# Optimization experiments

Hardware: AMD Instinct MI355X
Metric: run time of the kernel (lower is better)

The kernel has to match this reference:

```python
import jax, jax.numpy as jnp
import numpy as np

D_MODEL, D_FF = 1024, 4096
B, T = 4, 2048
K = 614  # int(d_ff * 0.15)


def setup_inputs() -> dict:
    key = jax.random.key(0)
    k1, k2, k3, k4 = jax.random.split(key, 4)
    s_in = 1.0 / np.sqrt(D_MODEL)
    s_ff = 1.0 / np.sqrt(D_FF)
    x = jax.random.normal(k1, (B, T, D_MODEL), jnp.float32)
    # torch nn.Linear default init: U(-1/sqrt(fan_in), 1/sqrt(fan_in)); weight shape [out, in]
    W1 = jax.random.uniform(k2, (D_FF, D_MODEL), jnp.float32, -s_in, s_in)
    W2 = jax.random.uniform(k3, (D_FF, D_MODEL), jnp.float32, -s_in, s_in)
    Wo = jax.random.uniform(k4, (D_MODEL, D_FF), jnp.float32, -s_ff, s_ff)
    return {"x": x, "W1": W1, "W2": W2, "Wo": Wo, "k": K}


def reference(x, W1, W2, Wo, k):
    gate = jnp.einsum('btd,fd->btf', x, W2)                 # [B,T,D_FF]
    act = jax.nn.silu(jnp.einsum('btd,fd->btf', x, W1))     # [B,T,D_FF]
    Bx, Tx, Dff = act.shape
    flat = act.reshape(Bx * Tx, Dff)
    _, topk_idx = jax.lax.top_k(flat, k)                    # [N, k]
    rows = jnp.arange(Bx * Tx)[:, None]
    mask = jnp.zeros_like(flat).at[rows, topk_idx].set(1.0).reshape(act.shape)
    sparse_act = act * mask                                  # eval-mode exact masking
    return jnp.einsum('btf,df->btd', sparse_act * gate, Wo)  # [B,T,D_MODEL]
```

## Files before the change

kernel.cpp:

```cpp
#include <hip/hip_runtime.h>
#include <stdint.h>

#define DEV __device__ __forceinline__

using f32x4  = __attribute__((ext_vector_type(4))) float;
using bf16x8 = __attribute__((ext_vector_type(8))) short;
typedef unsigned short u16;
typedef unsigned int   u32;

typedef const __attribute__((address_space(1))) void* gptr_t;
typedef __attribute__((address_space(3))) void*       lptr_t;

DEV u16 f2bf(float f) {
  union { float f; u32 u; } v; v.f = f;
  u32 lsb = (v.u >> 16) & 1u;
  v.u += 0x7fffu + lsb;
  return (u16)(v.u >> 16);
}
DEV float bf2f(u16 h) {
  union { u32 u; float f; } v; v.u = ((u32)h) << 16;
  return v.f;
}
DEV void async16(void* lds, const void* g) {
  __builtin_amdgcn_global_load_lds((gptr_t)(uintptr_t)g,
                                   (lptr_t)(u32)(uintptr_t)lds, 16, 0, 0);
}
DEV u32 fkey(float v) {
  u32 u = __float_as_uint(v);
  return u ^ ((u & 0x80000000u) ? 0xFFFFFFFFu : 0x80000000u);
}
DEV float unfkey(u32 key) {
  const u32 ub = (key & 0x80000000u) ? (key ^ 0x80000000u) : ~key;
  return __uint_as_float(ub);
}

__global__ __launch_bounds__(256) void splitall_kernel(
    const float* __restrict__ x,  const float* __restrict__ W1,
    const float* __restrict__ W2, const float* __restrict__ Wo,
    u16* __restrict__ x_hi, u16* __restrict__ x_lo,
    u16* __restrict__ W1h,  u16* __restrict__ W1l,
    u16* __restrict__ W2h,  u16* __restrict__ Woh,
    int nX, int nW, int nWo)
{
  const int i = blockIdx.x * 256 + threadIdx.x;
  const int total = nX + 2 * nW + nWo;
  if (i >= total) return;
  if (i < nX) {
    const float v = x[i];
    const u16 h = f2bf(v);
    x_hi[i] = h; x_lo[i] = f2bf(v - bf2f(h));
  } else if (i < nX + nW) {
    const int j = i - nX;
    const float v = W1[j];
    const u16 h = f2bf(v);
    W1h[j] = h; W1l[j] = f2bf(v - bf2f(h));
  } else if (i < nX + 2 * nW) {
    const int j = i - nX - nW;
    W2h[j] = f2bf(W2[j]);
  } else {
    const int j = i - nX - 2 * nW;
    Woh[j] = f2bf(Wo[j]);
  }
}

DEV void swz_block(int& bx, int& by) {
  const int gx = gridDim.x, nwg = gx * gridDim.y;
  const int lid = by * gx + bx;
  const int cpx = nwg >> 3;
  const int swz = (lid & 7) * cpx + (lid >> 3);
  bx = swz % gx; by = swz / gx;
}

template<int K, int NSEG, bool OUTBF16>
__global__ __launch_bounds__(512, 2) void gemm8p_kernel(
    const u16* __restrict__ A0, const u16* __restrict__ A1, const u16* __restrict__ A2,
    const u16* __restrict__ B0, const u16* __restrict__ B1, const u16* __restrict__ B2,
    void* __restrict__ Cout, int N)
{
  __shared__ u16 smem[65536];

  const int tid  = threadIdx.x;
  const int lane = tid & 63;
  const int wid  = tid >> 6;
  const int wm = wid >> 2, wn = wid & 3;
  int bx = blockIdx.x, by = blockIdx.y;
  swz_block(bx, by);
  const int m0 = by * 256, n0 = bx * 256;
  constexpr int TPS    = K >> 6;
  constexpr int nTiles = NSEG * TPS;
  constexpr int nIter  = nTiles / 2;

  f32x4 acc[8][4] = {};
  bf16x8 afr[4][2], bfr[2][2];

  auto stageHT = [&](int ab, int buf, int half, int ktile) {
    const int kt  = ktile < nTiles ? ktile : nTiles - 1;
    const int seg = kt / TPS;
    const int k0  = (kt - seg * TPS) << 6;
    const u16* __restrict__ src =
        ab ? (seg == 0 ? B0 : seg == 1 ? B1 : B2)
           : (seg == 0 ? A0 : seg == 1 ? A1 : A2);
    const int g0 = (ab ? n0 : m0) + half * 128;
    const int baseu = ((buf * 2 + ab) * 2 + half) * 8192;
#pragma unroll
    for (int L = 0; L < 2; ++L) {
      const int s = L * 512 + tid;
      const int r = s >> 3, cs = s & 7;
      const int csg = cs ^ (r & 7);
      async16(smem + baseu + (L * 512 + (tid & ~63)) * 8,
              src + (size_t)(g0 + r) * K + k0 + csg * 8);
    }
  };
  auto ldA = [&](int buf, int mi, int ks) -> bf16x8 {
    const int rA = wm * 128 + mi * 16 + (lane & 15);
    const int h = rA >> 7, rl = rA & 127;
    const int cs = (ks * 4 + (lane >> 4)) ^ (rl & 7);
    return *(const bf16x8*)&smem[((buf * 2 + 0) * 2 + h) * 8192 + rl * 64 + cs * 8];
  };
  auto ldB = [&](int buf, int ni, int ks) -> bf16x8 {
    const int rB = wn * 64 + ni * 16 + (lane & 15);
    const int h = rB >> 7, rl = rB & 127;
    const int cs = (ks * 4 + (lane >> 4)) ^ (rl & 7);
    return *(const bf16x8*)&smem[((buf * 2 + 1) * 2 + h) * 8192 + rl * 64 + cs * 8];
  };

  stageHT(0, 0, 0, 0); stageHT(0, 0, 1, 0);
  stageHT(1, 0, 0, 0); stageHT(1, 0, 1, 0);
  asm volatile("s_waitcnt vmcnt(0)" ::: "memory");
  __builtin_amdgcn_sched_barrier(0);
  __builtin_amdgcn_s_barrier();
  __builtin_amdgcn_sched_barrier(0);

  for (int i = 0; i < nIter; ++i) {
    const int t2 = 2 * i;
#pragma unroll
    for (int p = 0; p < 8; ++p) {
      const int pm = p & 3, bufC = p >> 2;
      const int miB = (pm >> 1) * 4, niB = (pm & 1) * 2;
      if ((pm & 1) == 0) {
#pragma unroll
        for (int m = 0; m < 4; ++m)
#pragma unroll
          for (int ks = 0; ks < 2; ++ks)
            afr[m][ks] = ldA(bufC, miB + m, ks);
      }
#pragma unroll
      for (int n = 0; n < 2; ++n)
#pragma unroll
        for (int ks = 0; ks < 2; ++ks)
          bfr[n][ks] = ldB(bufC, niB + n, ks);
      if (p == 0)      { stageHT(0, 1, 0, t2 + 1); stageHT(0, 1, 1, t2 + 1); }
      else if (p == 1) { stageHT(1, 1, 0, t2 + 1); stageHT(1, 1, 1, t2 + 1); }
      else if (p == 4) { stageHT(0, 0, 0, t2 + 2); stageHT(0, 0, 1, t2 + 2); }
      else if (p == 5) { stageHT(1, 0, 0, t2 + 2); stageHT(1, 0, 1, t2 + 2); }
      __builtin_amdgcn_sched_barrier(0);
      __builtin_amdgcn_s_barrier();
      __builtin_amdgcn_sched_barrier(0);
      __builtin_amdgcn_s_setprio(1);
#pragma unroll
      for (int m = 0; m < 4; ++m)
#pragma unroll
        for (int n = 0; n < 2; ++n)
#pragma unroll
          for (int ks = 0; ks < 2; ++ks)
            acc[miB + m][niB + n] = __builtin_amdgcn_mfma_f32_16x16x32_bf16(
                afr[m][ks], bfr[n][ks], acc[miB + m][niB + n], 0, 0, 0);
      __builtin_amdgcn_s_setprio(0);
      if (pm == 3)
        asm volatile("s_waitcnt vmcnt(0)" ::: "memory");
      __builtin_amdgcn_sched_barrier(0);
      __builtin_amdgcn_s_barrier();
      __builtin_amdgcn_sched_barrier(0);
    }
  }
  asm volatile("s_waitcnt vmcnt(0)" ::: "memory");

#pragma unroll
  for (int mi = 0; mi < 8; ++mi) {
    const int rb = m0 + wm * 128 + mi * 16 + (lane >> 4) * 4;
#pragma unroll
    for (int ni = 0; ni < 4; ++ni) {
      const int col = n0 + wn * 64 + ni * 16 + (lane & 15);
#pragma unroll
      for (int r2 = 0; r2 < 4; ++r2) {
        if constexpr (OUTBF16)
          ((u16*)Cout)[(size_t)(rb + r2) * N + col] = f2bf(acc[mi][ni][r2]);
        else
          ((float*)Cout)[(size_t)(rb + r2) * N + col] = acc[mi][ni][r2];
      }
    }
  }
}

template<int BK>
__global__ __launch_bounds__(256) void gemm_bt(
    const u16* __restrict__ A, const u16* __restrict__ B,
    float* __restrict__ C, int N, int K)
{
  constexpr int TILE = 128 * BK;
  __shared__ u16 smem[2 * TILE];
  u16* sA = smem;
  u16* sB = smem + TILE;

  const int tid  = threadIdx.x;
  const int lane = tid & 63;
  const int wave = tid >> 6;
  const int wr = wave >> 1, wc = wave & 1;
  int bx = blockIdx.x, by = blockIdx.y;
  swz_block(bx, by);
  const int m0 = by * 128, n0 = bx * 128;

  f32x4 acc[4][4] = {};
  constexpr int SPR   = BK / 8;
  constexpr int ITERS = (128 * SPR) / 256;

  for (int k0 = 0; k0 < K; k0 += BK) {
#pragma unroll
    for (int i = 0; i < ITERS; ++i) {
      const int slot = i * 256 + tid;
      const int r = slot / SPR, cc = slot % SPR;
      const int uni = (i * 256 + wave * 64) * 8;
      async16(sA + uni, A + (size_t)(m0 + r) * K + k0 + cc * 8);
      async16(sB + uni, B + (size_t)(n0 + r) * K + k0 + cc * 8);
    }
    __syncthreads();

#pragma unroll
    for (int ks = 0; ks < BK / 32; ++ks) {
      const int kb = ks * 32 + (lane >> 4) * 8;
      bf16x8 a[4], b[4];
#pragma unroll
      for (int i = 0; i < 4; ++i) {
        a[i] = *(const bf16x8*)&sA[(wr * 64 + i * 16 + (lane & 15)) * BK + kb];
        b[i] = *(const bf16x8*)&sB[(wc * 64 + i * 16 + (lane & 15)) * BK + kb];
      }
#pragma unroll
      for (int mi = 0; mi < 4; ++mi)
#pragma unroll
        for (int ni = 0; ni < 4; ++ni)
          acc[mi][ni] = __builtin_amdgcn_mfma_f32_16x16x32_bf16(a[mi], b[ni], acc[mi][ni], 0, 0, 0);
    }
    __syncthreads();
  }

#pragma unroll
  for (int mi = 0; mi < 4; ++mi) {
    const int rbase = m0 + wr * 64 + mi * 16 + (lane >> 4) * 4;
#pragma unroll
    for (int ni = 0; ni < 4; ++ni) {
      const int col = n0 + wc * 64 + ni * 16 + (lane & 15);
#pragma unroll
      for (int r2 = 0; r2 < 4; ++r2)
        C[(size_t)(rbase + r2) * N + col] = acc[mi][ni][r2];
    }
  }
}

__global__ __launch_bounds__(256) void select9_kernel(
    const float* __restrict__ z, u16* __restrict__ gs,
    const float* __restrict__ xin, const float* __restrict__ W1,
    const int* __restrict__ kptr)
{
  const int row = blockIdx.x, tid = threadIdx.x;
  const int lane = tid & 63, wave = tid >> 6;
  const int k = *kptr;

  __shared__ float xrow[1024];
  __shared__ float sact[4096];
  __shared__ unsigned char flag[4096];
  __shared__ int wsum[4];
  __shared__ int s_nb;
  __shared__ int band_idx[256];
  __shared__ u32 band_key[256];
  __shared__ float band_act[256];

  const float* zrow = z + (size_t)row * 4096;
  u16* gsrow = gs + (size_t)row * 4096;

  float zreg[16];
#pragma unroll
  for (int q = 0; q < 4; ++q) {
    const float4 v = *(const float4*)&zrow[q * 1024 + tid * 4];
    zreg[q * 4 + 0] = v.x; zreg[q * 4 + 1] = v.y;
    zreg[q * 4 + 2] = v.z; zreg[q * 4 + 3] = v.w;
  }
  *(float4*)&xrow[tid * 4] = *(const float4*)&xin[(size_t)row * 1024 + tid * 4];
  *(u32*)&flag[tid * 4] = 0u;
  *(u32*)&flag[1024 + tid * 4] = 0u;
  *(u32*)&flag[2048 + tid * 4] = 0u;
  *(u32*)&flag[3072 + tid * 4] = 0u;
  if (tid == 0) s_nb = 0;
  __syncthreads();

  u32 prefix = 0;
  for (int step = 0; step < 22; ++step) {
    const u32 c = prefix | (1u << (31 - step));
    const float zc = unfkey(c);
    int cnt = 0;
#pragma unroll
    for (int i = 0; i < 16; ++i) cnt += (zreg[i] >= zc) ? 1 : 0;
    for (int off = 32; off; off >>= 1) cnt += __shfl_xor(cnt, off);
    if (lane == 0) wsum[wave] = cnt;
    __syncthreads();
    const int tot = wsum[0] + wsum[1] + wsum[2] + wsum[3];
    if (tot >= k) prefix = c;
    __syncthreads();
  }
  const float tau = unfkey(prefix);
  const float BANDW = 8e-4f;
  const float thi = tau + BANDW, tlo = tau - BANDW;

  int cntD = 0;
#pragma unroll
  for (int q = 0; q < 4; ++q)
#pragma unroll
    for (int j = 0; j < 4; ++j) {
      const int f = q * 1024 + tid * 4 + j;
      const float zv = zreg[q * 4 + j];
      if (zv > thi) { flag[f] = 1; ++cntD; }
      else if (zv >= tlo) {
        const int p = atomicAdd(&s_nb, 1);
        if (p < 256) band_idx[p] = f;
      }
    }
  for (int off = 32; off; off >>= 1) cntD += __shfl_xor(cntD, off);
  if (lane == 0) wsum[wave] = cntD;
  __syncthreads();
  const int D = wsum[0] + wsum[1] + wsum[2] + wsum[3];
  const int nb = (s_nb < 256) ? s_nb : 256;
  const int need = k - D;

  {
    const int gi = tid >> 2, l = tid & 3;
    const int wl = lane & ~3;
    for (int i = gi; i < nb; i += 64) {
      const int f = band_idx[i];
      const float* wr = W1 + (size_t)f * 1024;
      float v = 0.f;
#pragma unroll 8
      for (int b = 0; b < 1024; b += 16) {
        float t = __fadd_rn(__fmul_rn(xrow[b + 12 + l], wr[b + 12 + l]), v);
        t = __fadd_rn(__fmul_rn(xrow[b + 8 + l],  wr[b + 8 + l]),  t);
        t = __fadd_rn(__fmul_rn(xrow[b + 4 + l],  wr[b + 4 + l]),  t);
        v = __fadd_rn(__fmul_rn(xrow[b + 0 + l],  wr[b + 0 + l]),  t);
      }
      const float c0 = __shfl(v, wl + 0);
      const float c1 = __shfl(v, wl + 1);
      const float c2 = __shfl(v, wl + 2);
      const float c3 = __shfl(v, wl + 3);
      if (l == 0) {
        const float zrep = __fadd_rn(__fadd_rn(c0, c1), __fadd_rn(c2, c3));
        const double zd = (double)zrep;
        const float a = (float)(zd / (1.0 + exp(-zd)));
        band_act[i] = a;
        band_key[i] = fkey(a);
      }
    }
  }
  __syncthreads();

  for (int i = tid; i < nb; i += 256) {
    const u32 ki = band_key[i];
    const int fi = band_idx[i];
    int rank = 0;
    for (int j = 0; j < nb; ++j) {
      const u32 kj = band_key[j];
      rank += (kj > ki || (kj == ki && band_idx[j] < fi)) ? 1 : 0;
    }
    if (rank < need) { flag[fi] = 2; sact[fi] = band_act[i]; }
  }
  __syncthreads();

#pragma unroll
  for (int q = 0; q < 4; ++q) {
    const int f0 = q * 1024 + tid * 4;
    const ushort4 gu = *(const ushort4*)&gsrow[f0];
    const float gvv[4] = { bf2f(gu.x), bf2f(gu.y), bf2f(gu.z), bf2f(gu.w) };
    const u32 fl = *(const u32*)&flag[f0];
    u16 out[4];
#pragma unroll
    for (int j = 0; j < 4; ++j) {
      const u32 fj = (fl >> (8 * j)) & 0xFF;
      float sval = 0.f;
      if (fj == 2) {
        sval = sact[f0 + j] * gvv[j];
      } else if (fj == 1) {
        const float zz = zreg[q * 4 + j];
        sval = (zz / (1.f + expf(-zz))) * gvv[j];
      }
      out[j] = f2bf(sval);
    }
    *(ushort4*)&gsrow[f0] = make_ushort4(out[0], out[1], out[2], out[3]);
  }
}

extern "C" void kernel_launch(void* const* d_in, const int* in_sizes, int n_in,
                              void* d_out, int out_size, void* d_ws, size_t ws_size,
                              hipStream_t stream)
{
  const float* x  = (const float*)d_in[0];
  const float* W1 = (const float*)d_in[1];
  const float* W2 = (const float*)d_in[2];
  const float* Wo = (const float*)d_in[3];
  const int* kptr = (const int*)d_in[4];

  const int DM = 1024, DF = 4096;
  const int M = in_sizes[0] / DM;
  const size_t nX = (size_t)M * DM, nW = (size_t)DF * DM, nWo = (size_t)DM * DF;

  char* w = (char*)d_ws;
  u16* x_hi  = (u16*)w;  w += nX * 2;
  u16* x_lo  = (u16*)w;  w += nX * 2;
  u16* W1_hi = (u16*)w;  w += nW * 2;
  u16* W1_lo = (u16*)w;  w += nW * 2;
  u16* W2_hi = (u16*)w;  w += nW * 2;
  u16* Wo_hi = (u16*)w;  w += nWo * 2;
  const size_t fixed_bytes = (size_t)(w - (char*)d_ws);

  int nch = 1;
  while (nch < 64) {
    const size_t per = (size_t)(M / nch) * DF * 6;
    if (fixed_bytes + per <= ws_size) break;
    nch *= 2;
  }
  const int Mc = M / nch;

  float* zbuf  = (float*)w;
  u16*   gsbuf = (u16*)(w + (size_t)Mc * DF * 4);

  {
    const long long total = (long long)nX + 2 * (long long)nW + (long long)nWo;
    splitall_kernel<<<dim3((int)((total + 255) / 256)), 256, 0, stream>>>(
        x, W1, W2, Wo, x_hi, x_lo, W1_hi, W1_lo, W2_hi, Wo_hi,
        (int)nX, (int)nW, (int)nWo);
  }

  for (int ch = 0; ch < nch; ++ch) {
    const size_t ro = (size_t)ch * Mc;
    gemm8p_kernel<1024, 3, false><<<dim3(DF / 256, Mc / 256), 512, 0, stream>>>(
        x_hi + ro * DM, x_hi + ro * DM, x_lo + ro * DM,
        W1_hi, W1_lo, W1_hi, zbuf, DF);
    gemm8p_kernel<1024, 1, true><<<dim3(DF / 256, Mc / 256), 512, 0, stream>>>(
        x_hi + ro * DM, x_hi + ro * DM, x_hi + ro * DM,
        W2_hi, W2_hi, W2_hi, gsbuf, DF);
    select9_kernel<<<dim3(Mc), 256, 0, stream>>>(
        zbuf, gsbuf, x + ro * DM, W1, kptr);
    gemm_bt<64><<<dim3(DM / 128, Mc / 128), 256, 0, stream>>>(
        gsbuf, Wo_hi, (float*)d_out + ro * DM, DM, DF);
  }
}
```

Measured before the change: 616.9 us.

## Merge z and gate GEMMs into one launch and vectorize split kernel

The two GEMM launches (the 3-segment split-precision z=x·W1 and the single-segment gate=x·W2) are combined into one grid, with the upper half of the y-blocks doing the gate work. This removes one launch and lets the short gate tiles fill the GPU alongside the longer z tiles, reducing tail idle time. The fp32-to-bf16 split kernel now works on float4/ushort4 vectors for wider memory accesses. The trade-off is a runtime nTiles and runtime pointer selection, which may cost some unrolling, and the swizzle now mixes blocks of unequal cost.

New measurement: 1.035 ms. +67.7%, slower.

```diff
diff --git a/kernel.cpp b/kernel.cpp
--- a/kernel.cpp
+++ b/kernel.cpp
@@ -40,26 +40,37 @@
     u16* __restrict__ x_hi, u16* __restrict__ x_lo,
     u16* __restrict__ W1h,  u16* __restrict__ W1l,
     u16* __restrict__ W2h,  u16* __restrict__ Woh,
-    int nX, int nW, int nWo)
+    int nX4, int nW4, int nWo4)
 {
-  const int i = blockIdx.x * 256 + threadIdx.x;
-  const int total = nX + 2 * nW + nWo;
-  if (i >= total) return;
-  if (i < nX) {
-    const float v = x[i];
-    const u16 h = f2bf(v);
-    x_hi[i] = h; x_lo[i] = f2bf(v - bf2f(h));
-  } else if (i < nX + nW) {
-    const int j = i - nX;
-    const float v = W1[j];
-    const u16 h = f2bf(v);
-    W1h[j] = h; W1l[j] = f2bf(v - bf2f(h));
-  } else if (i < nX + 2 * nW) {
-    const int j = i - nX - nW;
-    W2h[j] = f2bf(W2[j]);
+  const int i4 = blockIdx.x * 256 + threadIdx.x;
+  const int total4 = nX4 + 2 * nW4 + nWo4;
+  if (i4 >= total4) return;
+  if (i4 < nX4) {
+    const int j = i4 * 4;
+    const float4 v = *(const float4*)&x[j];
+    const float vv[4] = { v.x, v.y, v.z, v.w };
+    u16 h[4], l[4];
+#pragma unroll
+    for (int t = 0; t < 4; ++t) { h[t] = f2bf(vv[t]); l[t] = f2bf(vv[t] - bf2f(h[t])); }
+    *(ushort4*)&x_hi[j] = make_ushort4(h[0], h[1], h[2], h[3]);
+    *(ushort4*)&x_lo[j] = make_ushort4(l[0], l[1], l[2], l[3]);
+  } else if (i4 < nX4 + nW4) {
+    const int j = (i4 - nX4) * 4;
+    const float4 v = *(const float4*)&W1[j];
+    const float vv[4] = { v.x, v.y, v.z, v.w };
+    u16 h[4], l[4];
+#pragma unroll
+    for (int t = 0; t < 4; ++t) { h[t] = f2bf(vv[t]); l[t] = f2bf(vv[t] - bf2f(h[t])); }
+    *(ushort4*)&W1h[j] = make_ushort4(h[0], h[1], h[2], h[3]);
+    *(ushort4*)&W1l[j] = make_ushort4(l[0], l[1], l[2], l[3]);
+  } else if (i4 < nX4 + 2 * nW4) {
+    const int j = (i4 - nX4 - nW4) * 4;
+    const float4 v = *(const float4*)&W2[j];
+    *(ushort4*)&W2h[j] = make_ushort4(f2bf(v.x), f2bf(v.y), f2bf(v.z), f2bf(v.w));
   } else {
-    const int j = i - nX - 2 * nW;
-    Woh[j] = f2bf(Wo[j]);
+    const int j = (i4 - nX4 - 2 * nW4) * 4;
+    const float4 v = *(const float4*)&Wo[j];
+    *(ushort4*)&Woh[j] = make_ushort4(f2bf(v.x), f2bf(v.y), f2bf(v.z), f2bf(v.w));
   }
 }
 
@@ -71,11 +82,13 @@
   bx = swz % gx; by = swz / gx;
 }
 
-template<int K, int NSEG, bool OUTBF16>
-__global__ __launch_bounds__(512, 2) void gemm8p_kernel(
-    const u16* __restrict__ A0, const u16* __restrict__ A1, const u16* __restrict__ A2,
-    const u16* __restrict__ B0, const u16* __restrict__ B1, const u16* __restrict__ B2,
-    void* __restrict__ Cout, int N)
+template<int K>
+__global__ __launch_bounds__(512, 2) void gemmzg_kernel(
+    const u16* __restrict__ xh, const u16* __restrict__ xl,
+    const u16* __restrict__ W1h, const u16* __restrict__ W1l,
+    const u16* __restrict__ W2h,
+    float* __restrict__ zout, u16* __restrict__ gout,
+    int N, int mrows)
 {
   __shared__ u16 smem[65536];
 
@@ -85,10 +98,25 @@
   const int wm = wid >> 2, wn = wid & 3;
   int bx = blockIdx.x, by = blockIdx.y;
   swz_block(bx, by);
+
+  constexpr int TPS = K >> 6;
+  const u16 *A0, *A1, *A2, *B0, *B1, *B2;
+  int nTiles;
+  bool isZ;
+  if (by < mrows) {
+    isZ = true;
+    A0 = xh; A1 = xh; A2 = xl;
+    B0 = W1h; B1 = W1l; B2 = W1h;
+    nTiles = 3 * TPS;
+  } else {
+    isZ = false;
+    by -= mrows;
+    A0 = xh; A1 = xh; A2 = xh;
+    B0 = W2h; B1 = W2h; B2 = W2h;
+    nTiles = TPS;
+  }
   const int m0 = by * 256, n0 = bx * 256;
-  constexpr int TPS    = K >> 6;
-  constexpr int nTiles = NSEG * TPS;
-  constexpr int nIter  = nTiles / 2;
+  const int nIter = nTiles >> 1;
 
   f32x4 acc[8][4] = {};
   bf16x8 afr[4][2], bfr[2][2];
@@ -175,18 +203,28 @@
   }
   asm volatile("s_waitcnt vmcnt(0)" ::: "memory");
 
-#pragma unroll
-  for (int mi = 0; mi < 8; ++mi) {
-    const int rb = m0 + wm * 128 + mi * 16 + (lane >> 4) * 4;
-#pragma unroll
-    for (int ni = 0; ni < 4; ++ni) {
-      const int col = n0 + wn * 64 + ni * 16 + (lane & 15);
-#pragma unroll
-      for (int r2 = 0; r2 < 4; ++r2) {
-        if constexpr (OUTBF16)
-          ((u16*)Cout)[(size_t)(rb + r2) * N + col] = f2bf(acc[mi][ni][r2]);
-        else
-          ((float*)Cout)[(size_t)(rb + r2) * N + col] = acc[mi][ni][r2];
+  if (isZ) {
+#pragma unroll
+    for (int mi = 0; mi < 8; ++mi) {
+      const int rb = m0 + wm * 128 + mi * 16 + (lane >> 4) * 4;
+#pragma unroll
+      for (int ni = 0; ni < 4; ++ni) {
+        const int col = n0 + wn * 64 + ni * 16 + (lane & 15);
+#pragma unroll
+        for (int r2 = 0; r2 < 4; ++r2)
+          zout[(size_t)(rb + r2) * N + col] = acc[mi][ni][r2];
+      }
+    }
+  } else {
+#pragma unroll
+    for (int mi = 0; mi < 8; ++mi) {
+      const int rb = m0 + wm * 128 + mi * 16 + (lane >> 4) * 4;
+#pragma unroll
+      for (int ni = 0; ni < 4; ++ni) {
+        const int col = n0 + wn * 64 + ni * 16 + (lane & 15);
+#pragma unroll
+        for (int r2 = 0; r2 < 4; ++r2)
+          gout[(size_t)(rb + r2) * N + col] = f2bf(acc[mi][ni][r2]);
       }
     }
   }
@@ -429,20 +467,17 @@
   u16*   gsbuf = (u16*)(w + (size_t)Mc * DF * 4);
 
   {
-    const long long total = (long long)nX + 2 * (long long)nW + (long long)nWo;
-    splitall_kernel<<<dim3((int)((total + 255) / 256)), 256, 0, stream>>>(
+    const long long total4 = ((long long)nX + 2 * (long long)nW + (long long)nWo) / 4;
+    splitall_kernel<<<dim3((int)((total4 + 255) / 256)), 256, 0, stream>>>(
         x, W1, W2, Wo, x_hi, x_lo, W1_hi, W1_lo, W2_hi, Wo_hi,
-        (int)nX, (int)nW, (int)nWo);
+        (int)(nX / 4), (int)(nW / 4), (int)(nWo / 4));
   }
 
   for (int ch = 0; ch < nch; ++ch) {
     const size_t ro = (size_t)ch * Mc;
-    gemm8p_kernel<1024, 3, false><<<dim3(DF / 256, Mc / 256), 512, 0, stream>>>(
-        x_hi + ro * DM, x_hi + ro * DM, x_lo + ro * DM,
-        W1_hi, W1_lo, W1_hi, zbuf, DF);
-    gemm8p_kernel<1024, 1, true><<<dim3(DF / 256, Mc / 256), 512, 0, stream>>>(
-        x_hi + ro * DM, x_hi + ro * DM, x_hi + ro * DM,
-        W2_hi, W2_hi, W2_hi, gsbuf, DF);
+    gemmzg_kernel<1024><<<dim3(DF / 256, 2 * (Mc / 256)), 512, 0, stream>>>(
+        x_hi + ro * DM, x_lo + ro * DM, W1_hi, W1_lo, W2_hi,
+        zbuf, gsbuf, DF, Mc / 256);
     select9_kernel<<<dim3(Mc), 256, 0, stream>>>(
         zbuf, gsbuf, x + ro * DM, W1, kptr);
     gemm_bt<64><<<dim3(DM / 128, Mc / 128), 256, 0, stream>>>(
```
